# Optimization experiments

Measured on AMD Instinct MI355X. Metric: run time of the kernel, lower is better.

## Reference

```python
import jax, jax.numpy as jnp
import numpy as np

LATENT, HIDDEN, OUT, NBLOCKS, NITER, BATCH = 128, 256, 128, 4, 10, 65536

def setup_inputs() -> dict:
    key = jax.random.key(0)
    ks = jax.random.split(key, 7)
    s_in = 1.0 / np.sqrt(LATENT)
    s_h = 1.0 / np.sqrt(HIDDEN)
    return {
        "x": jax.random.normal(ks[0], (BATCH, LATENT), jnp.float32),
        "W_init": jax.random.uniform(ks[1], (LATENT, HIDDEN), jnp.float32, -s_in, s_in),
        "b_init": jnp.zeros((HIDDEN,), jnp.float32),
        "Wg1": jax.random.uniform(ks[2], (NBLOCKS, HIDDEN, HIDDEN), jnp.float32, -s_h, s_h),
        "bg1": jax.random.uniform(ks[3], (NBLOCKS, HIDDEN), jnp.float32, -s_h, s_h),
        "Wg2": jax.random.uniform(ks[4], (NBLOCKS, HIDDEN, HIDDEN), jnp.float32, -s_h, s_h),
        "bg2": jax.random.uniform(ks[5], (NBLOCKS, HIDDEN), jnp.float32, -s_h, s_h),
        "W_final": jax.random.uniform(ks[6], (HIDDEN, OUT), jnp.float32, -s_h, s_h),
        "b_final": jnp.zeros((OUT,), jnp.float32),
    }

def _block(y, W1, b1, W2, b2):
    # fixed-point iteration: x <- y - g(x), g = Linear-ReLU-Linear
    def step(x, _):
        g = jax.nn.relu(x @ W1 + b1) @ W2 + b2
        return y - g, None
    x, _ = jax.lax.scan(step, y, None, length=NITER)
    return x

def reference(x, W_init, b_init, Wg1, bg1, Wg2, bg2, W_final, b_final):
    h = x @ W_init + b_init  # [B, HIDDEN]
    def blk(h, params):
        W1, b1, W2, b2 = params
        return _block(h, W1, b1, W2, b2), None
    h, _ = jax.lax.scan(blk, h, (Wg1, bg1, Wg2, bg2))
    return h @ W_final + b_final
```

## Files before the change

kernel.cpp:

```cpp
#include <hip/hip_runtime.h>
#include <hip/hip_bf16.h>


#define B_TOTAL 65536
#define LATENT  128
#define HIDDEN  256
#define OUTD    128
#define NBLOCKS 4
#define NITER   10
#define MTILE   64
#define LDSP    264

typedef unsigned short u16;
typedef unsigned int   u32;
typedef u16    u16x4  __attribute__((ext_vector_type(4)));
typedef u16    u16x8  __attribute__((ext_vector_type(8)));
typedef __bf16 bf16x8 __attribute__((ext_vector_type(8)));
typedef float  f32x16 __attribute__((ext_vector_type(16)));

__device__ inline u16 f2b(float f){ __bf16 h=(__bf16)f; return __builtin_bit_cast(u16,h); }
__device__ inline float up_lo(u32 u){ return __builtin_bit_cast(float, u<<16); }
__device__ inline float up_hi(u32 u){ return __builtin_bit_cast(float, u & 0xffff0000u); }
__device__ inline u32 pk2(float lo, float hi){ return (u32)f2b(lo) | ((u32)f2b(hi)<<16); }

#define AGC \
 "a0","a1","a2","a3","a4","a5","a6","a7","a8","a9","a10","a11","a12","a13","a14","a15", \
 "a16","a17","a18","a19","a20","a21","a22","a23","a24","a25","a26","a27","a28","a29","a30","a31", \
 "a32","a33","a34","a35","a36","a37","a38","a39","a40","a41","a42","a43","a44","a45","a46","a47", \
 "a48","a49","a50","a51","a52","a53","a54","a55","a56","a57","a58","a59","a60","a61","a62","a63", \
 "a64","a65","a66","a67","a68","a69","a70","a71","a72","a73","a74","a75","a76","a77","a78","a79", \
 "a80","a81","a82","a83","a84","a85","a86","a87","a88","a89","a90","a91","a92","a93","a94","a95", \
 "a96","a97","a98","a99","a100","a101","a102","a103","a104","a105","a106","a107","a108","a109","a110","a111", \
 "a112","a113","a114","a115","a116","a117","a118","a119","a120","a121","a122","a123","a124","a125","a126","a127"

#define LOADW(P, KS, NEG, A0,A1,A2,A3) { \
  const float* _w = (P) + (size_t)((KS)*16 + hi*8)*HIDDEN + colw; \
  float _v0=_w[0], _v1=_w[HIDDEN], _v2=_w[2*HIDDEN], _v3=_w[3*HIDDEN]; \
  float _v4=_w[4*HIDDEN], _v5=_w[5*HIDDEN], _v6=_w[6*HIDDEN], _v7=_w[7*HIDDEN]; \
  if (NEG){_v0=-_v0;_v1=-_v1;_v2=-_v2;_v3=-_v3;_v4=-_v4;_v5=-_v5;_v6=-_v6;_v7=-_v7;} \
  u32 _d0=pk2(_v0,_v1), _d1=pk2(_v2,_v3), _d2=pk2(_v4,_v5), _d3=pk2(_v6,_v7); \
  asm volatile("v_accvgpr_write_b32 a" #A0 ", %0\n\t" \
               "v_accvgpr_write_b32 a" #A1 ", %1\n\t" \
               "v_accvgpr_write_b32 a" #A2 ", %2\n\t" \
               "v_accvgpr_write_b32 a" #A3 ", %3" \
               :: "v"(_d0),"v"(_d1),"v"(_d2),"v"(_d3) : AGC); }

#define STEP(SRC, KS, A0, A3) { \
  bf16x8 _b0 = *(const bf16x8*)((SRC) + rdA0 + (KS)*16); \
  bf16x8 _b1 = *(const bf16x8*)((SRC) + rdA1 + (KS)*16); \
  asm volatile("v_mfma_f32_32x32x16_bf16 %0, a[" #A0 ":" #A3 "], %1, %0" \
               : "+v"(acc0) : "v"(_b0) : AGC); \
  asm volatile("v_mfma_f32_32x32x16_bf16 %0, a[" #A0 ":" #A3 "], %1, %0" \
               : "+v"(acc1) : "v"(_b1) : AGC); }

#define ACCFENCE asm volatile("s_nop 7\n\ts_nop 7\n\ts_nop 7" : "+v"(acc0), "+v"(acc1))

#define MFMA_I(a,b,c) __builtin_amdgcn_mfma_f32_32x32x16_bf16(a,b,c,0,0,0)

__device__ inline bf16x8 load_wfrag_f(const float* __restrict__ W, int ldw, int krow0,
                                      int col){
  bf16x8 r;
#pragma unroll
  for (int j=0;j<8;j++) r[j] = (__bf16)W[(size_t)(krow0+j)*ldw + col];
  return r;
}

__device__ inline void store_tile(u16* __restrict__ dst, int row_elem, int nb, int hi,
                                  const f32x16 a, bool relu){
#pragma unroll
  for (int q=0;q<4;q++){
    u16x4 p;
#pragma unroll
    for (int i=0;i<4;i++){
      float v = a[4*q+i];
      if (relu) v = v > 0.f ? v : 0.f;
      p[i] = f2b(v);
    }
    *(u16x4*)(dst + row_elem + nb + 8*q + 4*hi) = p;
  }
}

__global__
__attribute__((amdgpu_flat_work_group_size(512,512)))
void irn_kernel(const float* __restrict__ x,
                const float* __restrict__ Winit, const float* __restrict__ binit,
                const float* __restrict__ Wg1,   const float* __restrict__ bg1,
                const float* __restrict__ Wg2,   const float* __restrict__ bg2,
                const float* __restrict__ Wfin,  const float* __restrict__ bfin,
                float* __restrict__ out)
{
  __shared__ u16 Xb[MTILE*LDSP];
  __shared__ u16 Hb[MTILE*LDSP];

  const int tid = threadIdx.x;
  const int wv  = tid >> 6;
  const int ln  = tid & 63;
  const int lo  = ln & 31;
  const int hi  = ln >> 5;
  const int row0 = blockIdx.x * MTILE;
  const int nb   = wv * 32;
  const int colw = nb + lo;

  {
    const int r  = tid >> 3;
    const int c0 = (tid & 7) * 16;
    const float4* src = (const float4*)(x + (size_t)(row0 + r)*LATENT + c0);
    u16x8 p0, p1;
#pragma unroll
    for (int i=0;i<2;i++){
      float4 a = src[i*2], b = src[i*2+1];
      u16x8& p = i ? p1 : p0;
      p[0]=f2b(a.x); p[1]=f2b(a.y); p[2]=f2b(a.z); p[3]=f2b(a.w);
      p[4]=f2b(b.x); p[5]=f2b(b.y); p[6]=f2b(b.z); p[7]=f2b(b.w);
    }
    u16* dst = Xb + r*LDSP + c0;
    *(u16x8*)(dst)   = p0;
    *(u16x8*)(dst+8) = p1;
  }

  const int rdA0 = lo*LDSP + hi*8;
  const int rdA1 = (32+lo)*LDSP + hi*8;

  u32 yp0[8], yp1[8];
  u32 b1p[8];

  __syncthreads();

  {
    bf16x8 wf[8];
#pragma unroll
    for (int ks=0; ks<8; ks++)
      wf[ks] = load_wfrag_f(Winit, HIDDEN, ks*16 + hi*8, colw);
    f32x16 acc0, acc1;
#pragma unroll
    for (int r=0;r<16;r++){
      float bv = binit[nb + (r&3) + 8*(r>>2) + 4*hi];
      acc0[r]=bv; acc1[r]=bv;
    }
#pragma unroll
    for (int ks=0; ks<8; ks++){
      bf16x8 b0 = *(const bf16x8*)(Xb + rdA0 + ks*16);
      bf16x8 b1 = *(const bf16x8*)(Xb + rdA1 + ks*16);
      acc0=MFMA_I(wf[ks], b0, acc0);
      acc1=MFMA_I(wf[ks], b1, acc1);
    }
    __syncthreads();
    store_tile(Xb, (0 +lo)*LDSP, nb, hi, acc0, false);
    store_tile(Xb, (32+lo)*LDSP, nb, hi, acc1, false);
#pragma unroll
    for (int i=0;i<8;i++){
      yp0[i] = pk2(acc0[2*i], acc0[2*i+1]);
      yp1[i] = pk2(acc1[2*i], acc1[2*i+1]);
    }
    __syncthreads();
  }

#pragma unroll 1
  for (int b=0; b<NBLOCKS; b++){
    const float* W1p = Wg1 + (size_t)b*HIDDEN*HIDDEN;
    const float* W2p = Wg2 + (size_t)b*HIDDEN*HIDDEN;

    LOADW(W1p, 0,0,  0,1,2,3)    LOADW(W1p, 1,0,  4,5,6,7)
    LOADW(W1p, 2,0,  8,9,10,11)  LOADW(W1p, 3,0,  12,13,14,15)
    LOADW(W1p, 4,0,  16,17,18,19) LOADW(W1p, 5,0,  20,21,22,23)
    LOADW(W1p, 6,0,  24,25,26,27) LOADW(W1p, 7,0,  28,29,30,31)
    LOADW(W1p, 8,0,  32,33,34,35) LOADW(W1p, 9,0,  36,37,38,39)
    LOADW(W1p,10,0,  40,41,42,43) LOADW(W1p,11,0,  44,45,46,47)
    LOADW(W1p,12,0,  48,49,50,51) LOADW(W1p,13,0,  52,53,54,55)
    LOADW(W1p,14,0,  56,57,58,59) LOADW(W1p,15,0,  60,61,62,63)
    LOADW(W2p, 0,1,  64,65,66,67)   LOADW(W2p, 1,1,  68,69,70,71)
    LOADW(W2p, 2,1,  72,73,74,75)   LOADW(W2p, 3,1,  76,77,78,79)
    LOADW(W2p, 4,1,  80,81,82,83)   LOADW(W2p, 5,1,  84,85,86,87)
    LOADW(W2p, 6,1,  88,89,90,91)   LOADW(W2p, 7,1,  92,93,94,95)
    LOADW(W2p, 8,1,  96,97,98,99)   LOADW(W2p, 9,1,  100,101,102,103)
    LOADW(W2p,10,1,  104,105,106,107) LOADW(W2p,11,1,  108,109,110,111)
    LOADW(W2p,12,1,  112,113,114,115) LOADW(W2p,13,1,  116,117,118,119)
    LOADW(W2p,14,1,  120,121,122,123) LOADW(W2p,15,1,  124,125,126,127)
    asm volatile("s_nop 3" :::);

    {
      const float* b1g = bg1 + b*HIDDEN;
      const float* b2g = bg2 + b*HIDDEN;
#pragma unroll
      for (int i=0;i<8;i++){
        const int c = nb + (2*i&3) + 8*(2*i>>2) + 4*hi;
        b1p[i] = pk2(b1g[c], b1g[c+1]);
        yp0[i] = pk2(up_lo(yp0[i]) - b2g[c], up_hi(yp0[i]) - b2g[c+1]);
        yp1[i] = pk2(up_lo(yp1[i]) - b2g[c], up_hi(yp1[i]) - b2g[c+1]);
      }
    }

#pragma unroll 1
    for (int it=0; it<NITER; it++){
      {
        f32x16 acc0, acc1;
#pragma unroll
        for (int i=0;i<8;i++){
          acc0[2*i]=up_lo(b1p[i]); acc0[2*i+1]=up_hi(b1p[i]);
          acc1[2*i]=acc0[2*i];     acc1[2*i+1]=acc0[2*i+1];
        }
        STEP(Xb, 0, 0,3)   STEP(Xb, 1, 4,7)   STEP(Xb, 2, 8,11)  STEP(Xb, 3, 12,15)
        STEP(Xb, 4, 16,19) STEP(Xb, 5, 20,23) STEP(Xb, 6, 24,27) STEP(Xb, 7, 28,31)
        STEP(Xb, 8, 32,35) STEP(Xb, 9, 36,39) STEP(Xb,10, 40,43) STEP(Xb,11, 44,47)
        STEP(Xb,12, 48,51) STEP(Xb,13, 52,55) STEP(Xb,14, 56,59) STEP(Xb,15, 60,63)
        ACCFENCE;
        store_tile(Hb, (0 +lo)*LDSP, nb, hi, acc0, true);
        store_tile(Hb, (32+lo)*LDSP, nb, hi, acc1, true);
      }
      __syncthreads();
      {
        f32x16 acc0, acc1;
#pragma unroll
        for (int i=0;i<8;i++){
          acc0[2*i]=up_lo(yp0[i]); acc0[2*i+1]=up_hi(yp0[i]);
          acc1[2*i]=up_lo(yp1[i]); acc1[2*i+1]=up_hi(yp1[i]);
        }
        STEP(Hb, 0, 64,67)   STEP(Hb, 1, 68,71)   STEP(Hb, 2, 72,75)   STEP(Hb, 3, 76,79)
        STEP(Hb, 4, 80,83)   STEP(Hb, 5, 84,87)   STEP(Hb, 6, 88,91)   STEP(Hb, 7, 92,95)
        STEP(Hb, 8, 96,99)   STEP(Hb, 9, 100,103) STEP(Hb,10, 104,107) STEP(Hb,11, 108,111)
        STEP(Hb,12, 112,115) STEP(Hb,13, 116,119) STEP(Hb,14, 120,123) STEP(Hb,15, 124,127)
        ACCFENCE;
        store_tile(Xb, (0 +lo)*LDSP, nb, hi, acc0, false);
        store_tile(Xb, (32+lo)*LDSP, nb, hi, acc1, false);
        if (it == NITER-1){
#pragma unroll
          for (int i=0;i<8;i++){
            yp0[i] = pk2(acc0[2*i], acc0[2*i+1]);
            yp1[i] = pk2(acc1[2*i], acc1[2*i+1]);
          }
        }
      }
      __syncthreads();
    }
  }

  {
    const int mf = (wv & 3) * 32;
    const int nf = (wv >> 2);
    const int rdF = (nf*32 + lo)*LDSP + hi*8;
    bf16x8 wf[16];
#pragma unroll
    for (int ks=0; ks<16; ks++)
      wf[ks] = load_wfrag_f(Wfin, OUTD, ks*16 + hi*8, mf + lo);
    f32x16 acc;
#pragma unroll
    for (int r=0;r<16;r++) acc[r] = bfin[mf + (r&3) + 8*(r>>2) + 4*hi];
#pragma unroll
    for (int ks=0; ks<16; ks++){
      bf16x8 bfr = *(const bf16x8*)(Xb + rdF + ks*16);
      acc = MFMA_I(wf[ks], bfr, acc);
    }
    float* orow = out + (size_t)(row0 + nf*32 + lo)*OUTD;
#pragma unroll
    for (int q=0;q<4;q++){
      float4 v = make_float4(acc[4*q], acc[4*q+1], acc[4*q+2], acc[4*q+3]);
      *(float4*)(orow + mf + 8*q + 4*hi) = v;
    }
  }
}

extern "C" void kernel_launch(void* const* d_in, const int* in_sizes, int n_in,
                              void* d_out, int out_size, void* d_ws, size_t ws_size,
                              hipStream_t stream) {
  (void)in_sizes; (void)n_in; (void)d_ws; (void)ws_size; (void)out_size;
  const float* x     = (const float*)d_in[0];
  const float* Winit = (const float*)d_in[1];
  const float* binit = (const float*)d_in[2];
  const float* Wg1   = (const float*)d_in[3];
  const float* bg1   = (const float*)d_in[4];
  const float* Wg2   = (const float*)d_in[5];
  const float* bg2   = (const float*)d_in[6];
  const float* Wfin  = (const float*)d_in[7];
  const float* bfin  = (const float*)d_in[8];
  float* out = (float*)d_out;
  irn_kernel<<<dim3(B_TOTAL/MTILE), dim3(512), 0, stream>>>(
      x, Winit, binit, Wg1, bg1, Wg2, bg2, Wfin, bfin, out);
}
```

Measured before the change: 777.5 us.

## Halve workgroup to 4 waves, each computing a 64-column tile with 256 AGPR weights

Workgroup size drops from 8 to 4 waves. Each wave now owns 64 output columns and keeps both W1 and W2 fragments for those columns resident in all 256 AGPRs. Every LDS B-fragment read now feeds two MFMAs instead of one, and the y residual stays in fp32 registers instead of packed bf16. The cost is one wave per SIMD (waves_per_eu 1), which leaves far less latency hiding, plus very high register pressure that could cause spills.

Result: slower. 960.0 us (+23.5%).

```diff
diff --git a/kernel.cpp b/kernel.cpp
--- a/kernel.cpp
+++ b/kernel.cpp
@@ -19,8 +19,6 @@
 typedef float  f32x16 __attribute__((ext_vector_type(16)));
 
 __device__ inline u16 f2b(float f){ __bf16 h=(__bf16)f; return __builtin_bit_cast(u16,h); }
-__device__ inline float up_lo(u32 u){ return __builtin_bit_cast(float, u<<16); }
-__device__ inline float up_hi(u32 u){ return __builtin_bit_cast(float, u & 0xffff0000u); }
 __device__ inline u32 pk2(float lo, float hi){ return (u32)f2b(lo) | ((u32)f2b(hi)<<16); }
 
 #define AGC \
@@ -31,10 +29,18 @@
  "a64","a65","a66","a67","a68","a69","a70","a71","a72","a73","a74","a75","a76","a77","a78","a79", \
  "a80","a81","a82","a83","a84","a85","a86","a87","a88","a89","a90","a91","a92","a93","a94","a95", \
  "a96","a97","a98","a99","a100","a101","a102","a103","a104","a105","a106","a107","a108","a109","a110","a111", \
- "a112","a113","a114","a115","a116","a117","a118","a119","a120","a121","a122","a123","a124","a125","a126","a127"
-
-#define LOADW(P, KS, NEG, A0,A1,A2,A3) { \
-  const float* _w = (P) + (size_t)((KS)*16 + hi*8)*HIDDEN + colw; \
+ "a112","a113","a114","a115","a116","a117","a118","a119","a120","a121","a122","a123","a124","a125","a126","a127", \
+ "a128","a129","a130","a131","a132","a133","a134","a135","a136","a137","a138","a139","a140","a141","a142","a143", \
+ "a144","a145","a146","a147","a148","a149","a150","a151","a152","a153","a154","a155","a156","a157","a158","a159", \
+ "a160","a161","a162","a163","a164","a165","a166","a167","a168","a169","a170","a171","a172","a173","a174","a175", \
+ "a176","a177","a178","a179","a180","a181","a182","a183","a184","a185","a186","a187","a188","a189","a190","a191", \
+ "a192","a193","a194","a195","a196","a197","a198","a199","a200","a201","a202","a203","a204","a205","a206","a207", \
+ "a208","a209","a210","a211","a212","a213","a214","a215","a216","a217","a218","a219","a220","a221","a222","a223", \
+ "a224","a225","a226","a227","a228","a229","a230","a231","a232","a233","a234","a235","a236","a237","a238","a239", \
+ "a240","a241","a242","a243","a244","a245","a246","a247","a248","a249","a250","a251","a252","a253","a254","a255"
+
+#define LOADW(P, KS, NEG, COL, A0,A1,A2,A3) { \
+  const float* _w = (P) + (size_t)((KS)*16 + hi*8)*HIDDEN + (COL); \
   float _v0=_w[0], _v1=_w[HIDDEN], _v2=_w[2*HIDDEN], _v3=_w[3*HIDDEN]; \
   float _v4=_w[4*HIDDEN], _v5=_w[5*HIDDEN], _v6=_w[6*HIDDEN], _v7=_w[7*HIDDEN]; \
   if (NEG){_v0=-_v0;_v1=-_v1;_v2=-_v2;_v3=-_v3;_v4=-_v4;_v5=-_v5;_v6=-_v6;_v7=-_v7;} \
@@ -45,15 +51,20 @@
                "v_accvgpr_write_b32 a" #A3 ", %3" \
                :: "v"(_d0),"v"(_d1),"v"(_d2),"v"(_d3) : AGC); }
 
-#define STEP(SRC, KS, A0, A3) { \
-  bf16x8 _b0 = *(const bf16x8*)((SRC) + rdA0 + (KS)*16); \
-  bf16x8 _b1 = *(const bf16x8*)((SRC) + rdA1 + (KS)*16); \
-  asm volatile("v_mfma_f32_32x32x16_bf16 %0, a[" #A0 ":" #A3 "], %1, %0" \
-               : "+v"(acc0) : "v"(_b0) : AGC); \
-  asm volatile("v_mfma_f32_32x32x16_bf16 %0, a[" #A0 ":" #A3 "], %1, %0" \
-               : "+v"(acc1) : "v"(_b1) : AGC); }
-
-#define ACCFENCE asm volatile("s_nop 7\n\ts_nop 7\n\ts_nop 7" : "+v"(acc0), "+v"(acc1))
+#define STEPX(SRC, KS, P,Q, R,S) { \
+  const int _off = rdA + (KS)*16; \
+  bf16x8 _b0 = *(const bf16x8*)((SRC) + _off); \
+  bf16x8 _b1 = *(const bf16x8*)((SRC) + 32*LDSP + _off); \
+  asm volatile("v_mfma_f32_32x32x16_bf16 %0, a[" #P ":" #Q "], %1, %0" : "+v"(acc00) : "v"(_b0) : AGC); \
+  asm volatile("v_mfma_f32_32x32x16_bf16 %0, a[" #P ":" #Q "], %1, %0" : "+v"(acc10) : "v"(_b1) : AGC); \
+  asm volatile("v_mfma_f32_32x32x16_bf16 %0, a[" #R ":" #S "], %1, %0" : "+v"(acc01) : "v"(_b0) : AGC); \
+  asm volatile("v_mfma_f32_32x32x16_bf16 %0, a[" #R ":" #S "], %1, %0" : "+v"(acc11) : "v"(_b1) : AGC); }
+
+#define ACCINIT_FENCE asm volatile("s_nop 2" \
+  : "+v"(acc00), "+v"(acc01), "+v"(acc10), "+v"(acc11))
+
+#define ACCFENCE asm volatile("s_nop 7\n\ts_nop 7\n\ts_nop 7" \
+  : "+v"(acc00), "+v"(acc01), "+v"(acc10), "+v"(acc11))
 
 #define MFMA_I(a,b,c) __builtin_amdgcn_mfma_f32_32x32x16_bf16(a,b,c,0,0,0)
 
@@ -65,7 +76,7 @@
   return r;
 }
 
-__device__ inline void store_tile(u16* __restrict__ dst, int row_elem, int nb, int hi,
+__device__ inline void store_tile(u16* __restrict__ dst, int row_elem, int colb,
                                   const f32x16 a, bool relu){
 #pragma unroll
   for (int q=0;q<4;q++){
@@ -76,12 +87,13 @@
       if (relu) v = v > 0.f ? v : 0.f;
       p[i] = f2b(v);
     }
-    *(u16x4*)(dst + row_elem + nb + 8*q + 4*hi) = p;
+    *(u16x4*)(dst + row_elem + colb + 8*q) = p;
   }
 }
 
 __global__
-__attribute__((amdgpu_flat_work_group_size(512,512)))
+__attribute__((amdgpu_flat_work_group_size(256,256)))
+__attribute__((amdgpu_waves_per_eu(1,1)))
 void irn_kernel(const float* __restrict__ x,
                 const float* __restrict__ Winit, const float* __restrict__ binit,
                 const float* __restrict__ Wg1,   const float* __restrict__ bg1,
@@ -98,60 +110,63 @@
   const int lo  = ln & 31;
   const int hi  = ln >> 5;
   const int row0 = blockIdx.x * MTILE;
-  const int nb   = wv * 32;
-  const int colw = nb + lo;
+  const int nb0  = wv * 64;
+  const int nb1  = nb0 + 32;
+  const int colw0 = nb0 + lo;
+  const int colw1 = nb1 + lo;
+
+  const int rdA = lo*LDSP + 8*hi;
+  const int cb0 = nb0 + 4*hi;
+  const int cb1 = nb1 + 4*hi;
 
   {
-    const int r  = tid >> 3;
-    const int c0 = (tid & 7) * 16;
+    const int r  = tid >> 2;
+    const int c0 = (tid & 3) * 32;
     const float4* src = (const float4*)(x + (size_t)(row0 + r)*LATENT + c0);
-    u16x8 p0, p1;
-#pragma unroll
-    for (int i=0;i<2;i++){
-      float4 a = src[i*2], b = src[i*2+1];
-      u16x8& p = i ? p1 : p0;
+#pragma unroll
+    for (int j=0;j<4;j++){
+      float4 a = src[2*j], b = src[2*j+1];
+      u16x8 p;
       p[0]=f2b(a.x); p[1]=f2b(a.y); p[2]=f2b(a.z); p[3]=f2b(a.w);
       p[4]=f2b(b.x); p[5]=f2b(b.y); p[6]=f2b(b.z); p[7]=f2b(b.w);
-    }
-    u16* dst = Xb + r*LDSP + c0;
-    *(u16x8*)(dst)   = p0;
-    *(u16x8*)(dst+8) = p1;
-  }
-
-  const int rdA0 = lo*LDSP + hi*8;
-  const int rdA1 = (32+lo)*LDSP + hi*8;
-
-  u32 yp0[8], yp1[8];
-  u32 b1p[8];
+      *(u16x8*)(Xb + r*LDSP + c0 + 8*j) = p;
+    }
+  }
+
+  f32x16 yv00, yv01, yv10, yv11;
 
   __syncthreads();
 
   {
-    bf16x8 wf[8];
-#pragma unroll
-    for (int ks=0; ks<8; ks++)
-      wf[ks] = load_wfrag_f(Winit, HIDDEN, ks*16 + hi*8, colw);
-    f32x16 acc0, acc1;
+    bf16x8 wf0[8], wf1[8];
+#pragma unroll
+    for (int ks=0; ks<8; ks++){
+      wf0[ks] = load_wfrag_f(Winit, HIDDEN, ks*16 + hi*8, colw0);
+      wf1[ks] = load_wfrag_f(Winit, HIDDEN, ks*16 + hi*8, colw1);
+    }
+    f32x16 acc00, acc01, acc10, acc11;
 #pragma unroll
     for (int r=0;r<16;r++){
-      float bv = binit[nb + (r&3) + 8*(r>>2) + 4*hi];
-      acc0[r]=bv; acc1[r]=bv;
+      const int c = (r&3) + 8*(r>>2) + 4*hi;
+      acc00[r]=binit[nb0+c]; acc01[r]=binit[nb1+c];
+      acc10[r]=acc00[r];     acc11[r]=acc01[r];
     }
 #pragma unroll
     for (int ks=0; ks<8; ks++){
-      bf16x8 b0 = *(const bf16x8*)(Xb + rdA0 + ks*16);
-      bf16x8 b1 = *(const bf16x8*)(Xb + rdA1 + ks*16);
-      acc0=MFMA_I(wf[ks], b0, acc0);
-      acc1=MFMA_I(wf[ks], b1, acc1);
+      const int off = rdA + ks*16;
+      bf16x8 b0 = *(const bf16x8*)(Xb + off);
+      bf16x8 b1 = *(const bf16x8*)(Xb + 32*LDSP + off);
+      acc00=MFMA_I(wf0[ks], b0, acc00);
+      acc10=MFMA_I(wf0[ks], b1, acc10);
+      acc01=MFMA_I(wf1[ks], b0, acc01);
+      acc11=MFMA_I(wf1[ks], b1, acc11);
     }
     __syncthreads();
-    store_tile(Xb, (0 +lo)*LDSP, nb, hi, acc0, false);
-    store_tile(Xb, (32+lo)*LDSP, nb, hi, acc1, false);
-#pragma unroll
-    for (int i=0;i<8;i++){
-      yp0[i] = pk2(acc0[2*i], acc0[2*i+1]);
-      yp1[i] = pk2(acc1[2*i], acc1[2*i+1]);
-    }
+    store_tile(Xb, (0 +lo)*LDSP, cb0, acc00, false);
+    store_tile(Xb, (0 +lo)*LDSP, cb1, acc01, false);
+    store_tile(Xb, (32+lo)*LDSP, cb0, acc10, false);
+    store_tile(Xb, (32+lo)*LDSP, cb1, acc11, false);
+    yv00=acc00; yv01=acc01; yv10=acc10; yv11=acc11;
     __syncthreads();
   }
 
@@ -160,101 +175,122 @@
     const float* W1p = Wg1 + (size_t)b*HIDDEN*HIDDEN;
     const float* W2p = Wg2 + (size_t)b*HIDDEN*HIDDEN;
 
-    LOADW(W1p, 0,0,  0,1,2,3)    LOADW(W1p, 1,0,  4,5,6,7)
-    LOADW(W1p, 2,0,  8,9,10,11)  LOADW(W1p, 3,0,  12,13,14,15)
-    LOADW(W1p, 4,0,  16,17,18,19) LOADW(W1p, 5,0,  20,21,22,23)
-    LOADW(W1p, 6,0,  24,25,26,27) LOADW(W1p, 7,0,  28,29,30,31)
-    LOADW(W1p, 8,0,  32,33,34,35) LOADW(W1p, 9,0,  36,37,38,39)
-    LOADW(W1p,10,0,  40,41,42,43) LOADW(W1p,11,0,  44,45,46,47)
-    LOADW(W1p,12,0,  48,49,50,51) LOADW(W1p,13,0,  52,53,54,55)
-    LOADW(W1p,14,0,  56,57,58,59) LOADW(W1p,15,0,  60,61,62,63)
-    LOADW(W2p, 0,1,  64,65,66,67)   LOADW(W2p, 1,1,  68,69,70,71)
-    LOADW(W2p, 2,1,  72,73,74,75)   LOADW(W2p, 3,1,  76,77,78,79)
-    LOADW(W2p, 4,1,  80,81,82,83)   LOADW(W2p, 5,1,  84,85,86,87)
-    LOADW(W2p, 6,1,  88,89,90,91)   LOADW(W2p, 7,1,  92,93,94,95)
-    LOADW(W2p, 8,1,  96,97,98,99)   LOADW(W2p, 9,1,  100,101,102,103)
-    LOADW(W2p,10,1,  104,105,106,107) LOADW(W2p,11,1,  108,109,110,111)
-    LOADW(W2p,12,1,  112,113,114,115) LOADW(W2p,13,1,  116,117,118,119)
-    LOADW(W2p,14,1,  120,121,122,123) LOADW(W2p,15,1,  124,125,126,127)
+    LOADW(W1p, 0,0,colw0,  0,1,2,3)     LOADW(W1p, 1,0,colw0,  4,5,6,7)
+    LOADW(W1p, 2,0,colw0,  8,9,10,11)   LOADW(W1p, 3,0,colw0,  12,13,14,15)
+    LOADW(W1p, 4,0,colw0,  16,17,18,19) LOADW(W1p, 5,0,colw0,  20,21,22,23)
+    LOADW(W1p, 6,0,colw0,  24,25,26,27) LOADW(W1p, 7,0,colw0,  28,29,30,31)
+    LOADW(W1p, 8,0,colw0,  32,33,34,35) LOADW(W1p, 9,0,colw0,  36,37,38,39)
+    LOADW(W1p,10,0,colw0,  40,41,42,43) LOADW(W1p,11,0,colw0,  44,45,46,47)
+    LOADW(W1p,12,0,colw0,  48,49,50,51) LOADW(W1p,13,0,colw0,  52,53,54,55)
+    LOADW(W1p,14,0,colw0,  56,57,58,59) LOADW(W1p,15,0,colw0,  60,61,62,63)
+    LOADW(W1p, 0,0,colw1,  64,65,66,67)     LOADW(W1p, 1,0,colw1,  68,69,70,71)
+    LOADW(W1p, 2,0,colw1,  72,73,74,75)     LOADW(W1p, 3,0,colw1,  76,77,78,79)
+    LOADW(W1p, 4,0,colw1,  80,81,82,83)     LOADW(W1p, 5,0,colw1,  84,85,86,87)
+    LOADW(W1p, 6,0,colw1,  88,89,90,91)     LOADW(W1p, 7,0,colw1,  92,93,94,95)
+    LOADW(W1p, 8,0,colw1,  96,97,98,99)     LOADW(W1p, 9,0,colw1,  100,101,102,103)
+    LOADW(W1p,10,0,colw1,  104,105,106,107) LOADW(W1p,11,0,colw1,  108,109,110,111)
+    LOADW(W1p,12,0,colw1,  112,113,114,115) LOADW(W1p,13,0,colw1,  116,117,118,119)
+    LOADW(W1p,14,0,colw1,  120,121,122,123) LOADW(W1p,15,0,colw1,  124,125,126,127)
+    LOADW(W2p, 0,1,colw0,  128,129,130,131) LOADW(W2p, 1,1,colw0,  132,133,134,135)
+    LOADW(W2p, 2,1,colw0,  136,137,138,139) LOADW(W2p, 3,1,colw0,  140,141,142,143)
+    LOADW(W2p, 4,1,colw0,  144,145,146,147) LOADW(W2p, 5,1,colw0,  148,149,150,151)
+    LOADW(W2p, 6,1,colw0,  152,153,154,155) LOADW(W2p, 7,1,colw0,  156,157,158,159)
+    LOADW(W2p, 8,1,colw0,  160,161,162,163) LOADW(W2p, 9,1,colw0,  164,165,166,167)
+    LOADW(W2p,10,1,colw0,  168,169,170,171) LOADW(W2p,11,1,colw0,  172,173,174,175)
+    LOADW(W2p,12,1,colw0,  176,177,178,179) LOADW(W2p,13,1,colw0,  180,181,182,183)
+    LOADW(W2p,14,1,colw0,  184,185,186,187) LOADW(W2p,15,1,colw0,  188,189,190,191)
+    LOADW(W2p, 0,1,colw1,  192,193,194,195) LOADW(W2p, 1,1,colw1,  196,197,198,199)
+    LOADW(W2p, 2,1,colw1,  200,201,202,203) LOADW(W2p, 3,1,colw1,  204,205,206,207)
+    LOADW(W2p, 4,1,colw1,  208,209,210,211) LOADW(W2p, 5,1,colw1,  212,213,214,215)
+    LOADW(W2p, 6,1,colw1,  216,217,218,219) LOADW(W2p, 7,1,colw1,  220,221,222,223)
+    LOADW(W2p, 8,1,colw1,  224,225,226,227) LOADW(W2p, 9,1,colw1,  228,229,230,231)
+    LOADW(W2p,10,1,colw1,  232,233,234,235) LOADW(W2p,11,1,colw1,  236,237,238,239)
+    LOADW(W2p,12,1,colw1,  240,241,242,243) LOADW(W2p,13,1,colw1,  244,245,246,247)
+    LOADW(W2p,14,1,colw1,  248,249,250,251) LOADW(W2p,15,1,colw1,  252,253,254,255)
     asm volatile("s_nop 3" :::);
 
+    f32x16 b1v0, b1v1;
     {
       const float* b1g = bg1 + b*HIDDEN;
       const float* b2g = bg2 + b*HIDDEN;
 #pragma unroll
-      for (int i=0;i<8;i++){
-        const int c = nb + (2*i&3) + 8*(2*i>>2) + 4*hi;
-        b1p[i] = pk2(b1g[c], b1g[c+1]);
-        yp0[i] = pk2(up_lo(yp0[i]) - b2g[c], up_hi(yp0[i]) - b2g[c+1]);
-        yp1[i] = pk2(up_lo(yp1[i]) - b2g[c], up_hi(yp1[i]) - b2g[c+1]);
+      for (int r=0;r<16;r++){
+        const int c = (r&3) + 8*(r>>2) + 4*hi;
+        b1v0[r] = b1g[nb0+c];  b1v1[r] = b1g[nb1+c];
+        const float b20 = b2g[nb0+c], b21 = b2g[nb1+c];
+        yv00[r] -= b20; yv10[r] -= b20;
+        yv01[r] -= b21; yv11[r] -= b21;
       }
     }
 
 #pragma unroll 1
     for (int it=0; it<NITER; it++){
       {
-        f32x16 acc0, acc1;
-#pragma unroll
-        for (int i=0;i<8;i++){
-          acc0[2*i]=up_lo(b1p[i]); acc0[2*i+1]=up_hi(b1p[i]);
-          acc1[2*i]=acc0[2*i];     acc1[2*i+1]=acc0[2*i+1];
-        }
-        STEP(Xb, 0, 0,3)   STEP(Xb, 1, 4,7)   STEP(Xb, 2, 8,11)  STEP(Xb, 3, 12,15)
-        STEP(Xb, 4, 16,19) STEP(Xb, 5, 20,23) STEP(Xb, 6, 24,27) STEP(Xb, 7, 28,31)
-        STEP(Xb, 8, 32,35) STEP(Xb, 9, 36,39) STEP(Xb,10, 40,43) STEP(Xb,11, 44,47)
-        STEP(Xb,12, 48,51) STEP(Xb,13, 52,55) STEP(Xb,14, 56,59) STEP(Xb,15, 60,63)
+        f32x16 acc00=b1v0, acc01=b1v1, acc10=b1v0, acc11=b1v1;
+        ACCINIT_FENCE;
+        STEPX(Xb, 0,  0,3,   64,67)   STEPX(Xb, 1,  4,7,   68,71)
+        STEPX(Xb, 2,  8,11,  72,75)   STEPX(Xb, 3,  12,15, 76,79)
+        STEPX(Xb, 4,  16,19, 80,83)   STEPX(Xb, 5,  20,23, 84,87)
+        STEPX(Xb, 6,  24,27, 88,91)   STEPX(Xb, 7,  28,31, 92,95)
+        STEPX(Xb, 8,  32,35, 96,99)   STEPX(Xb, 9,  36,39, 100,103)
+        STEPX(Xb,10,  40,43, 104,107) STEPX(Xb,11,  44,47, 108,111)
+        STEPX(Xb,12,  48,51, 112,115) STEPX(Xb,13,  52,55, 116,119)
+        STEPX(Xb,14,  56,59, 120,123) STEPX(Xb,15,  60,63, 124,127)
         ACCFENCE;
-        store_tile(Hb, (0 +lo)*LDSP, nb, hi, acc0, true);
-        store_tile(Hb, (32+lo)*LDSP, nb, hi, acc1, true);
+        store_tile(Hb, (0 +lo)*LDSP, cb0, acc00, true);
+        store_tile(Hb, (0 +lo)*LDSP, cb1, acc01, true);
+        store_tile(Hb, (32+lo)*LDSP, cb0, acc10, true);
+        store_tile(Hb, (32+lo)*LDSP, cb1, acc11, true);
       }
       __syncthreads();
       {
-        f32x16 acc0, acc1;
-#pragma unroll
-        for (int i=0;i<8;i++){
-          acc0[2*i]=up_lo(yp0[i]); acc0[2*i+1]=up_hi(yp0[i]);
-          acc1[2*i]=up_lo(yp1[i]); acc1[2*i+1]=up_hi(yp1[i]);
-        }
-        STEP(Hb, 0, 64,67)   STEP(Hb, 1, 68,71)   STEP(Hb, 2, 72,75)   STEP(Hb, 3, 76,79)
-        STEP(Hb, 4, 80,83)   STEP(Hb, 5, 84,87)   STEP(Hb, 6, 88,91)   STEP(Hb, 7, 92,95)
-        STEP(Hb, 8, 96,99)   STEP(Hb, 9, 100,103) STEP(Hb,10, 104,107) STEP(Hb,11, 108,111)
-        STEP(Hb,12, 112,115) STEP(Hb,13, 116,119) STEP(Hb,14, 120,123) STEP(Hb,15, 124,127)
+        f32x16 acc00=yv00, acc01=yv01, acc10=yv10, acc11=yv11;
+        ACCINIT_FENCE;
+        STEPX(Hb, 0,  128,131, 192,195) STEPX(Hb, 1,  132,135, 196,199)
+        STEPX(Hb, 2,  136,139, 200,203) STEPX(Hb, 3,  140,143, 204,207)
+        STEPX(Hb, 4,  144,147, 208,211) STEPX(Hb, 5,  148,151, 212,215)
+        STEPX(Hb, 6,  152,155, 216,219) STEPX(Hb, 7,  156,159, 220,223)
+        STEPX(Hb, 8,  160,163, 224,227) STEPX(Hb, 9,  164,167, 228,231)
+        STEPX(Hb,10,  168,171, 232,235) STEPX(Hb,11,  172,175, 236,239)
+        STEPX(Hb,12,  176,179, 240,243) STEPX(Hb,13,  180,183, 244,247)
+        STEPX(Hb,14,  184,187, 248,251) STEPX(Hb,15,  188,191, 252,255)
         ACCFENCE;
-        store_tile(Xb, (0 +lo)*LDSP, nb, hi, acc0, false);
-        store_tile(Xb, (32+lo)*LDSP, nb, hi, acc1, false);
-        if (it == NITER-1){
-#pragma unroll
-          for (int i=0;i<8;i++){
-            yp0[i] = pk2(acc0[2*i], acc0[2*i+1]);
-            yp1[i] = pk2(acc1[2*i], acc1[2*i+1]);
-          }
-        }
+        store_tile(Xb, (0 +lo)*LDSP, cb0, acc00, false);
+        store_tile(Xb, (0 +lo)*LDSP, cb1, acc01, false);
+        store_tile(Xb, (32+lo)*LDSP, cb0, acc10, false);
+        store_tile(Xb, (32+lo)*LDSP, cb1, acc11, false);
+        if (it == NITER-1){ yv00=acc00; yv01=acc01; yv10=acc10; yv11=acc11; }
       }
       __syncthreads();
     }
   }
 
   {
-    const int mf = (wv & 3) * 32;
-    const int nf = (wv >> 2);
-    const int rdF = (nf*32 + lo)*LDSP + hi*8;
+    const int colf = wv*32 + lo;
     bf16x8 wf[16];
 #pragma unroll
     for (int ks=0; ks<16; ks++)
-      wf[ks] = load_wfrag_f(Wfin, OUTD, ks*16 + hi*8, mf + lo);
-    f32x16 acc;
-#pragma unroll
-    for (int r=0;r<16;r++) acc[r] = bfin[mf + (r&3) + 8*(r>>2) + 4*hi];
+      wf[ks] = load_wfrag_f(Wfin, OUTD, ks*16 + hi*8, colf);
+    f32x16 acc0, acc1;
+#pragma unroll
+    for (int r=0;r<16;r++){
+      const float bv = bfin[wv*32 + (r&3) + 8*(r>>2) + 4*hi];
+      acc0[r]=bv; acc1[r]=bv;
+    }
 #pragma unroll
     for (int ks=0; ks<16; ks++){
-      bf16x8 bfr = *(const bf16x8*)(Xb + rdF + ks*16);
-      acc = MFMA_I(wf[ks], bfr, acc);
-    }
-    float* orow = out + (size_t)(row0 + nf*32 + lo)*OUTD;
+      const int off = rdA + ks*16;
+      bf16x8 b0 = *(const bf16x8*)(Xb + off);
+      bf16x8 b1 = *(const bf16x8*)(Xb + 32*LDSP + off);
+      acc0 = MFMA_I(wf[ks], b0, acc0);
+      acc1 = MFMA_I(wf[ks], b1, acc1);
+    }
+    float* orow0 = out + (size_t)(row0 + lo)*OUTD + wv*32;
+    float* orow1 = out + (size_t)(row0 + 32 + lo)*OUTD + wv*32;
 #pragma unroll
     for (int q=0;q<4;q++){
-      float4 v = make_float4(acc[4*q], acc[4*q+1], acc[4*q+2], acc[4*q+3]);
-      *(float4*)(orow + mf + 8*q + 4*hi) = v;
+      *(float4*)(orow0 + 8*q + 4*hi) = make_float4(acc0[4*q],acc0[4*q+1],acc0[4*q+2],acc0[4*q+3]);
+      *(float4*)(orow1 + 8*q + 4*hi) = make_float4(acc1[4*q],acc1[4*q+1],acc1[4*q+2],acc1[4*q+3]);
     }
   }
 }
@@ -273,6 +309,6 @@
   const float* Wfin  = (const float*)d_in[7];
   const float* bfin  = (const float*)d_in[8];
   float* out = (float*)d_out;
-  irn_kernel<<<dim3(B_TOTAL/MTILE), dim3(512), 0, stream>>>(
+  irn_kernel<<<dim3(B_TOTAL/MTILE), dim3(256), 0, stream>>>(
       x, Winit, binit, Wg1, bg1, Wg2, bg2, Wfin, bfin, out);
 }
```
